# Kernel tuning notes

Hardware: AMD Instinct MI355X
Metric: run time of the kernel (lower is better)

Reference implementation:

```python
import jax, jax.numpy as jnp
import numpy as np
import math

B, H, S, D = 2, 16, 2048, 64


def setup_inputs() -> dict:
    key = jax.random.key(0)
    kq, kk, kv, km = jax.random.split(key, 4)
    query = jax.random.normal(kq, (B, H, S, D), dtype=jnp.float32)
    k_ = jax.random.normal(kk, (B, H, S, D), dtype=jnp.float32)
    value = jax.random.normal(kv, (B, H, S, D), dtype=jnp.float32)
    mask = jax.random.randint(km, (B, 1, S, S), 0, 2).astype(jnp.bool_)
    return {"query": query, "key": k_, "value": value, "mask": mask}


def reference(query, key, value, mask):
    d = query.shape[-1]
    # scores: [B, H, S, S]
    scores = jnp.einsum("bhqd,bhkd->bhqk", query, key) / math.sqrt(d)
    scores = jnp.clip(scores, 1e-09, 1e9)
    # bool-mask branch of the original: masked_fill(mask == False, -1e9)
    scores = jnp.where(mask, scores, jnp.float32(-1e9))
    p_attn = jax.nn.softmax(scores, axis=-1)
    out = jnp.einsum("bhqk,bhkd->bhqd", p_attn, value)
    return out, p_attn
```

## Files before the change

### kernel.cpp

```cpp
#include <hip/hip_runtime.h>


#define B_ 2
#define H_ 16
#define S_ 2048
#define D_ 64
#define BQ 64
#define NQT (S_ / BQ)
#define NCH (S_ / 64)

typedef __attribute__((ext_vector_type(8))) short bf16x8;
typedef __attribute__((ext_vector_type(4))) float f32x4;

__device__ inline short f2bf(float f) {
    unsigned u = __float_as_uint(f);
    u = (u + 0x7FFFu + ((u >> 16) & 1u)) >> 16;
    return (short)u;
}

__device__ __forceinline__ void loadRM(const float* __restrict__ src, int tid, float4* r) {
#pragma unroll
    for (int it = 0; it < 2; ++it) {
        const int g = it * 256 + tid;
        const float4* s4 = reinterpret_cast<const float4*>(src + (g >> 3) * 64 + (g & 7) * 8);
        r[it * 2]     = s4[0];
        r[it * 2 + 1] = s4[1];
    }
}
__device__ __forceinline__ void writeRM(short* dst, int tid, const float4* r) {
#pragma unroll
    for (int it = 0; it < 2; ++it) {
        const int g = it * 256 + tid;
        const int row = g >> 3, b = g & 7;
        const float4 a = r[it * 2], c = r[it * 2 + 1];
        bf16x8 v;
        v[0]=f2bf(a.x); v[1]=f2bf(a.y); v[2]=f2bf(a.z); v[3]=f2bf(a.w);
        v[4]=f2bf(c.x); v[5]=f2bf(c.y); v[6]=f2bf(c.z); v[7]=f2bf(c.w);
        *reinterpret_cast<bf16x8*>(&dst[row * 64 + ((b ^ (row & 7)) << 3)]) = v;
    }
}
__device__ __forceinline__ void loadVc(const float* __restrict__ src, int tid, float* vr) {
    const int d = tid & 63, kq = tid >> 6;
#pragma unroll
    for (int i = 0; i < 16; ++i)
        vr[i] = src[(size_t)(kq * 16 + i) * 64 + d];
}
__device__ __forceinline__ void writeVc(short* dst, int tid, const float* vr) {
    const int d = tid & 63, kq = tid >> 6;
#pragma unroll
    for (int h = 0; h < 2; ++h) {
        bf16x8 v;
#pragma unroll
        for (int i = 0; i < 8; ++i) v[i] = f2bf(vr[h * 8 + i]);
        *reinterpret_cast<bf16x8*>(&dst[d * 64 + (((2 * kq + h) ^ (d & 7)) << 3)]) = v;
    }
}

#define BODY_A(CH, CUR, MVC, MVN)                                              \
  {                                                                            \
    const int ch_ = (CH);                                                      \
    if (ch_ + 1 < NCH) {                                                       \
      _Pragma("unroll") for (int kc = 0; kc < 4; ++kc)                         \
      _Pragma("unroll") for (int j = 0; j < 4; ++j)                            \
        MVN[kc*4+j] = Mb[mrow0 + (size_t)j*S_ + (size_t)(ch_+1)*64 + kc*16 + c16]; \
    }                                                                          \
    __builtin_amdgcn_s_setprio(1);                                             \
    _Pragma("unroll") for (int kc = 0; kc < 4; ++kc) {                         \
      const int kr = kc*16 + c16;                                              \
      bf16x8 kf0 = *(const bf16x8*)&Ks[CUR][kr*64 + ((g16 ^ rsw) << 3)];       \
      bf16x8 kf1 = *(const bf16x8*)&Ks[CUR][kr*64 + (((4+g16) ^ rsw) << 3)];   \
      f32x4 acc = {0.f,0.f,0.f,0.f};                                           \
      acc = __builtin_amdgcn_mfma_f32_16x16x32_bf16(qf0, kf0, acc, 0,0,0);     \
      acc = __builtin_amdgcn_mfma_f32_16x16x32_bf16(qf1, kf1, acc, 0,0,0);     \
      _Pragma("unroll") for (int j = 0; j < 4; ++j) {                          \
        float s = acc[j] * 0.125f;                                             \
        s = fminf(fmaxf(s, 1e-9f), 1e9f);                                      \
        const float e = MVC[kc*4+j] ? __expf(s) : 0.f;                         \
        esum[j] += e;                                                          \
        const int row = g16*4 + j, cg = kc*16 + c16;                           \
        Ps[wv][row*64 + ((cg & 7) | (((cg >> 3) ^ (row & 7)) << 3))] = f2bf(e);\
      }                                                                        \
    }                                                                          \
    _Pragma("unroll") for (int ks = 0; ks < 2; ++ks) {                         \
      bf16x8 pa = *(const bf16x8*)&Ps[wv][c16*64 + (((ks*4+g16) ^ rsw) << 3)]; \
      _Pragma("unroll") for (int dt = 0; dt < 4; ++dt) {                       \
        const int vr_ = dt*16 + c16;                                           \
        bf16x8 vb = *(const bf16x8*)&Vs[CUR][vr_*64 + (((ks*4+g16) ^ (vr_ & 7)) << 3)]; \
        o[dt] = __builtin_amdgcn_mfma_f32_16x16x32_bf16(pa, vb, o[dt], 0,0,0); \
      }                                                                        \
    }                                                                          \
    __builtin_amdgcn_s_setprio(0);                                             \
    {                                                                          \
      unsigned wb = 0;                                                         \
      _Pragma("unroll") for (int i = 0; i < 16; ++i)                           \
        wb |= (MVC[i] != 0 ? 1u : 0u) << i;                                    \
      MBh[tid * 34 + ch_] = (unsigned short)wb;                                \
    }                                                                          \
    if (ch_ + 1 < NCH) { writeRM(Ks[(CUR)^1], tid, kA); writeVc(Vs[(CUR)^1], tid, vA); } \
    if (ch_ + 2 < NCH) { loadRM(Kb + (size_t)(ch_+2)*4096, tid, kA);           \
                         loadVc(Vb + (size_t)(ch_+2)*4096, tid, vA); }         \
    __syncthreads();                                                           \
  }

#define BODY_B(CH, CUR, MKW)                                                   \
  {                                                                            \
    const int ch_ = (CH);                                                      \
    const unsigned mw_ = (MKW);                                                \
    __builtin_amdgcn_s_setprio(1);                                             \
    _Pragma("unroll") for (int kc = 0; kc < 4; ++kc) {                         \
      const int kr = kc*16 + c16;                                              \
      bf16x8 kf0 = *(const bf16x8*)&Ks[CUR][kr*64 + ((g16 ^ rsw) << 3)];       \
      bf16x8 kf1 = *(const bf16x8*)&Ks[CUR][kr*64 + (((4+g16) ^ rsw) << 3)];   \
      f32x4 acc = {0.f,0.f,0.f,0.f};                                           \
      acc = __builtin_amdgcn_mfma_f32_16x16x32_bf16(qf0, kf0, acc, 0,0,0);     \
      acc = __builtin_amdgcn_mfma_f32_16x16x32_bf16(qf1, kf1, acc, 0,0,0);     \
      _Pragma("unroll") for (int j = 0; j < 4; ++j) {                          \
        float s = acc[j] * 0.125f;                                             \
        s = fminf(fmaxf(s, 1e-9f), 1e9f);                                      \
        const float p = ((mw_ >> (kc*4 + j)) & 1u) ? __expf(s) * inv[j] : 0.f; \
        Pg[(size_t)(wv*16 + g16*4 + j)*S_ + (size_t)ch_*64 + kc*16 + c16] = p; \
      }                                                                        \
    }                                                                          \
    __builtin_amdgcn_s_setprio(0);                                             \
    if (ch_ + 1 < NCH) writeRM(Ks[(CUR)^1], tid, kA);                          \
    if (ch_ + 2 < NCH) loadRM(Kb + (size_t)(ch_+2)*4096, tid, kA);             \
    __syncthreads();                                                           \
  }

__global__ __launch_bounds__(256, 2) void attn_fused(
    const float* __restrict__ Q, const float* __restrict__ K,
    const float* __restrict__ V, const int* __restrict__ M,
    float* __restrict__ Out, float* __restrict__ P)
{
    __shared__ short Ks[2][4096];
    __shared__ short Vs[2][4096];
    __shared__ short Ps[4][1024];
    __shared__ unsigned short MBh[256 * 34];

    const int tid  = threadIdx.x;
    const int wv   = tid >> 6;
    const int lane = tid & 63;
    const int g16  = lane >> 4;
    const int c16  = lane & 15;
    const int rsw  = c16 & 7;

    const int wid = (blockIdx.x & 7) * (gridDim.x >> 3) + (blockIdx.x >> 3);
    const int bh = wid >> 5;
    const int qt = wid & 31;
    const int qbase = qt * BQ;

    const float* Qb = Q + ((size_t)bh * S_ + qbase) * D_;
    const float* Kb = K + (size_t)bh * S_ * D_;
    const float* Vb = V + (size_t)bh * S_ * D_;
    const int*   Mb = M + (size_t)(bh >> 4) * S_ * S_;
    float*       Pg = P + ((size_t)bh * S_ + qbase) * S_;
    float*       Og = Out + ((size_t)bh * S_ + qbase) * D_;

    float4 kA[4]; float vA[16];

    {
        float4 qA[4];
        loadRM(Qb, tid, qA);
        loadRM(Kb, tid, kA);
        loadVc(Vb, tid, vA);
        writeRM(&Ps[0][0], tid, qA);
    }
    __syncthreads();
    const int qrow = wv * 16 + c16;
    const short* Qst = &Ps[0][0];
    const bf16x8 qf0 = *(const bf16x8*)&Qst[qrow*64 + ((g16 ^ rsw) << 3)];
    const bf16x8 qf1 = *(const bf16x8*)&Qst[qrow*64 + (((4+g16) ^ rsw) << 3)];
    writeRM(Ks[0], tid, kA);
    writeVc(Vs[0], tid, vA);
    loadRM(Kb + 4096, tid, kA);
    loadVc(Vb + 4096, tid, vA);

    const size_t mrow0 = (size_t)(qbase + wv*16 + g16*4) * S_;
    int mv0[16], mv1[16];
#pragma unroll
    for (int kc = 0; kc < 4; ++kc)
#pragma unroll
        for (int j = 0; j < 4; ++j)
            mv0[kc*4+j] = Mb[mrow0 + (size_t)j*S_ + kc*16 + c16];
    __syncthreads();

    float esum[4] = {0.f, 0.f, 0.f, 0.f};
    f32x4 o[4];
#pragma unroll
    for (int dt = 0; dt < 4; ++dt) o[dt] = f32x4{0.f, 0.f, 0.f, 0.f};

    for (int t = 0; t < NCH/2; ++t) {
        BODY_A(2*t,     0, mv0, mv1)
        BODY_A(2*t + 1, 1, mv1, mv0)
    }

    float inv[4];
#pragma unroll
    for (int j = 0; j < 4; ++j) {
        float v = esum[j];
        v += __shfl_xor(v, 1);
        v += __shfl_xor(v, 2);
        v += __shfl_xor(v, 4);
        v += __shfl_xor(v, 8);
        inv[j] = 1.0f / v;
    }
#pragma unroll
    for (int dt = 0; dt < 4; ++dt)
#pragma unroll
        for (int j = 0; j < 4; ++j)
            Og[(size_t)(wv*16 + g16*4 + j) * D_ + dt*16 + c16] = o[dt][j] * inv[j];

    loadRM(Kb, tid, kA);
    writeRM(Ks[0], tid, kA);
    loadRM(Kb + 4096, tid, kA);
    __syncthreads();

    for (int t = 0; t < NCH/2; ++t) {
        const unsigned w = *(const unsigned*)&MBh[tid * 34 + 2*t];
        BODY_B(2*t,     0, w & 0xffffu)
        BODY_B(2*t + 1, 1, w >> 16)
    }
}

extern "C" void kernel_launch(void* const* d_in, const int* in_sizes, int n_in,
                              void* d_out, int out_size, void* d_ws, size_t ws_size,
                              hipStream_t stream) {
    const float* Q = (const float*)d_in[0];
    const float* K = (const float*)d_in[1];
    const float* V = (const float*)d_in[2];
    const int*   M = (const int*)d_in[3];

    float* Out = (float*)d_out;
    float* P   = (float*)d_out + (size_t)B_ * H_ * S_ * D_;

    hipLaunchKernelGGL(attn_fused, dim3(B_ * H_ * NQT), dim3(256), 0, stream,
                       Q, K, V, M, Out, P);
}
```

Measured before the change: 249.3 us.

## Precompute packed mask bitmask in workspace before fused attention kernel

Adds a pre-pass kernel that packs the int mask into 64-bit ballot words in the workspace. The attention kernel then reads these compact words instead of re-reading int32 mask values from every head's block, and drops the shared-memory mask-bit cache. That cache took about 17KB of LDS, so the launch bound rises to allow 3 blocks per CU. The cost is an extra kernel launch and a full pass over the mask, and a fallback to the old kernel remains when the workspace is too small.

```diff
diff --git a/kernel.cpp b/kernel.cpp
--- a/kernel.cpp
+++ b/kernel.cpp
@@ -8,9 +8,11 @@
 #define BQ 64
 #define NQT (S_ / BQ)
 #define NCH (S_ / 64)
+#define BM_WORDS ((size_t)B_ * S_ * (S_ / 64))
 
 typedef __attribute__((ext_vector_type(8))) short bf16x8;
 typedef __attribute__((ext_vector_type(4))) float f32x4;
+typedef unsigned long long u64;
 
 __device__ inline short f2bf(float f) {
     unsigned u = __float_as_uint(f);
@@ -56,7 +58,178 @@
     }
 }
 
-#define BODY_A(CH, CUR, MVC, MVN)                                              \
+__global__ __launch_bounds__(256, 8) void build_bitmask_ws(const int* __restrict__ M,
+                                                           u64* __restrict__ BM)
+{
+    const unsigned total = (unsigned)B_ * S_ * S_;
+    const unsigned stride = gridDim.x * 256;
+    for (unsigned i = blockIdx.x * 256 + threadIdx.x; i < total; i += stride) {
+        const bool mk = (M[i] != 0);
+        const u64 bal = __ballot(mk);
+        if ((threadIdx.x & 63) == 0) BM[i >> 6] = bal;
+    }
+}
+
+#define BODY_A(CH, CUR, BMC, BMN)                                              \
+  {                                                                            \
+    const int ch_ = (CH);                                                      \
+    if (ch_ + 1 < NCH) {                                                       \
+      _Pragma("unroll") for (int j = 0; j < 4; ++j)                            \
+        BMN[j] = BM[Lbase + (size_t)j * 32 + (ch_ + 1)];                       \
+    }                                                                          \
+    __builtin_amdgcn_s_setprio(1);                                             \
+    _Pragma("unroll") for (int kc = 0; kc < 4; ++kc) {                         \
+      const int kr = kc*16 + c16;                                              \
+      bf16x8 kf0 = *(const bf16x8*)&Ks[CUR][kr*64 + ((g16 ^ rsw) << 3)];       \
+      bf16x8 kf1 = *(const bf16x8*)&Ks[CUR][kr*64 + (((4+g16) ^ rsw) << 3)];   \
+      f32x4 acc = {0.f,0.f,0.f,0.f};                                           \
+      acc = __builtin_amdgcn_mfma_f32_16x16x32_bf16(qf0, kf0, acc, 0,0,0);     \
+      acc = __builtin_amdgcn_mfma_f32_16x16x32_bf16(qf1, kf1, acc, 0,0,0);     \
+      _Pragma("unroll") for (int j = 0; j < 4; ++j) {                          \
+        float s = acc[j] * 0.125f;                                             \
+        s = fminf(fmaxf(s, 1e-9f), 1e9f);                                      \
+        const float e = ((BMC[j] >> (kc*16 + c16)) & 1ULL) ? __expf(s) : 0.f;  \
+        esum[j] += e;                                                          \
+        const int row = g16*4 + j, cg = kc*16 + c16;                           \
+        Ps[wv][row*64 + ((cg & 7) | (((cg >> 3) ^ (row & 7)) << 3))] = f2bf(e);\
+      }                                                                        \
+    }                                                                          \
+    _Pragma("unroll") for (int ks = 0; ks < 2; ++ks) {                         \
+      bf16x8 pa = *(const bf16x8*)&Ps[wv][c16*64 + (((ks*4+g16) ^ rsw) << 3)]; \
+      _Pragma("unroll") for (int dt = 0; dt < 4; ++dt) {                       \
+        const int vr_ = dt*16 + c16;                                           \
+        bf16x8 vb = *(const bf16x8*)&Vs[CUR][vr_*64 + (((ks*4+g16) ^ (vr_ & 7)) << 3)]; \
+        o[dt] = __builtin_amdgcn_mfma_f32_16x16x32_bf16(pa, vb, o[dt], 0,0,0); \
+      }                                                                        \
+    }                                                                          \
+    __builtin_amdgcn_s_setprio(0);                                             \
+    if (ch_ + 1 < NCH) { writeRM(Ks[(CUR)^1], tid, kA); writeVc(Vs[(CUR)^1], tid, vA); } \
+    if (ch_ + 2 < NCH) { loadRM(Kb + (size_t)(ch_+2)*4096, tid, kA);           \
+                         loadVc(Vb + (size_t)(ch_+2)*4096, tid, vA); }         \
+    __syncthreads();                                                           \
+  }
+
+#define BODY_B(CH, CUR, BMC, BMN)                                              \
+  {                                                                            \
+    const int ch_ = (CH);                                                      \
+    if (ch_ + 1 < NCH) {                                                       \
+      _Pragma("unroll") for (int j = 0; j < 4; ++j)                            \
+        BMN[j] = BM[Lbase + (size_t)j * 32 + (ch_ + 1)];                       \
+    }                                                                          \
+    __builtin_amdgcn_s_setprio(1);                                             \
+    _Pragma("unroll") for (int kc = 0; kc < 4; ++kc) {                         \
+      const int kr = kc*16 + c16;                                              \
+      bf16x8 kf0 = *(const bf16x8*)&Ks[CUR][kr*64 + ((g16 ^ rsw) << 3)];       \
+      bf16x8 kf1 = *(const bf16x8*)&Ks[CUR][kr*64 + (((4+g16) ^ rsw) << 3)];   \
+      f32x4 acc = {0.f,0.f,0.f,0.f};                                           \
+      acc = __builtin_amdgcn_mfma_f32_16x16x32_bf16(qf0, kf0, acc, 0,0,0);     \
+      acc = __builtin_amdgcn_mfma_f32_16x16x32_bf16(qf1, kf1, acc, 0,0,0);     \
+      _Pragma("unroll") for (int j = 0; j < 4; ++j) {                          \
+        float s = acc[j] * 0.125f;                                             \
+        s = fminf(fmaxf(s, 1e-9f), 1e9f);                                      \
+        const float p = ((BMC[j] >> (kc*16 + c16)) & 1ULL) ? __expf(s)*inv[j] : 0.f; \
+        Pg[(size_t)(wv*16 + g16*4 + j)*S_ + (size_t)ch_*64 + kc*16 + c16] = p; \
+      }                                                                        \
+    }                                                                          \
+    __builtin_amdgcn_s_setprio(0);                                             \
+    if (ch_ + 1 < NCH) writeRM(Ks[(CUR)^1], tid, kA);                          \
+    if (ch_ + 2 < NCH) loadRM(Kb + (size_t)(ch_+2)*4096, tid, kA);             \
+    __syncthreads();                                                           \
+  }
+
+__global__ __launch_bounds__(256, 3) void attn_bm(
+    const float* __restrict__ Q, const float* __restrict__ K,
+    const float* __restrict__ V, const u64* __restrict__ BM,
+    float* __restrict__ Out, float* __restrict__ P)
+{
+    __shared__ short Ks[2][4096];
+    __shared__ short Vs[2][4096];
+    __shared__ short Ps[4][1024];
+
+    const int tid  = threadIdx.x;
+    const int wv   = tid >> 6;
+    const int lane = tid & 63;
+    const int g16  = lane >> 4;
+    const int c16  = lane & 15;
+    const int rsw  = c16 & 7;
+
+    const int wid = (blockIdx.x & 7) * (gridDim.x >> 3) + (blockIdx.x >> 3);
+    const int bh = wid >> 5;
+    const int qt = wid & 31;
+    const int qbase = qt * BQ;
+
+    const float* Qb = Q + ((size_t)bh * S_ + qbase) * D_;
+    const float* Kb = K + (size_t)bh * S_ * D_;
+    const float* Vb = V + (size_t)bh * S_ * D_;
+    float*       Pg = P + ((size_t)bh * S_ + qbase) * S_;
+    float*       Og = Out + ((size_t)bh * S_ + qbase) * D_;
+
+    const size_t Lbase = ((size_t)(bh >> 4) * S_ + qbase + wv*16 + g16*4) * 32;
+
+    float4 kA[4]; float vA[16];
+
+    {
+        float4 qA[4];
+        loadRM(Qb, tid, qA);
+        loadRM(Kb, tid, kA);
+        loadVc(Vb, tid, vA);
+        writeRM(&Ps[0][0], tid, qA);
+    }
+    __syncthreads();
+    const int qrow = wv * 16 + c16;
+    const short* Qst = &Ps[0][0];
+    const bf16x8 qf0 = *(const bf16x8*)&Qst[qrow*64 + ((g16 ^ rsw) << 3)];
+    const bf16x8 qf1 = *(const bf16x8*)&Qst[qrow*64 + (((4+g16) ^ rsw) << 3)];
+    writeRM(Ks[0], tid, kA);
+    writeVc(Vs[0], tid, vA);
+    loadRM(Kb + 4096, tid, kA);
+    loadVc(Vb + 4096, tid, vA);
+
+    u64 bm0[4], bm1[4];
+#pragma unroll
+    for (int j = 0; j < 4; ++j) bm0[j] = BM[Lbase + (size_t)j * 32];
+    __syncthreads();
+
+    float esum[4] = {0.f, 0.f, 0.f, 0.f};
+    f32x4 o[4];
+#pragma unroll
+    for (int dt = 0; dt < 4; ++dt) o[dt] = f32x4{0.f, 0.f, 0.f, 0.f};
+
+    for (int t = 0; t < NCH/2; ++t) {
+        BODY_A(2*t,     0, bm0, bm1)
+        BODY_A(2*t + 1, 1, bm1, bm0)
+    }
+
+    float inv[4];
+#pragma unroll
+    for (int j = 0; j < 4; ++j) {
+        float v = esum[j];
+        v += __shfl_xor(v, 1);
+        v += __shfl_xor(v, 2);
+        v += __shfl_xor(v, 4);
+        v += __shfl_xor(v, 8);
+        inv[j] = 1.0f / v;
+    }
+#pragma unroll
+    for (int dt = 0; dt < 4; ++dt)
+#pragma unroll
+        for (int j = 0; j < 4; ++j)
+            Og[(size_t)(wv*16 + g16*4 + j) * D_ + dt*16 + c16] = o[dt][j] * inv[j];
+
+    loadRM(Kb, tid, kA);
+#pragma unroll
+    for (int j = 0; j < 4; ++j) bm0[j] = BM[Lbase + (size_t)j * 32];
+    writeRM(Ks[0], tid, kA);
+    loadRM(Kb + 4096, tid, kA);
+    __syncthreads();
+
+    for (int t = 0; t < NCH/2; ++t) {
+        BODY_B(2*t,     0, bm0, bm1)
+        BODY_B(2*t + 1, 1, bm1, bm0)
+    }
+}
+
+#define BODY_AR(CH, CUR, MVC, MVN)                                             \
   {                                                                            \
     const int ch_ = (CH);                                                      \
     if (ch_ + 1 < NCH) {                                                       \
@@ -102,7 +275,7 @@
     __syncthreads();                                                           \
   }
 
-#define BODY_B(CH, CUR, MKW)                                                   \
+#define BODY_BR(CH, CUR, MKW)                                                  \
   {                                                                            \
     const int ch_ = (CH);                                                      \
     const unsigned mw_ = (MKW);                                                \
@@ -127,7 +300,7 @@
     __syncthreads();                                                           \
   }
 
-__global__ __launch_bounds__(256, 2) void attn_fused(
+__global__ __launch_bounds__(256, 2) void attn_fused_raw(
     const float* __restrict__ Q, const float* __restrict__ K,
     const float* __restrict__ V, const int* __restrict__ M,
     float* __restrict__ Out, float* __restrict__ P)
@@ -157,7 +330,6 @@
     float*       Og = Out + ((size_t)bh * S_ + qbase) * D_;
 
     float4 kA[4]; float vA[16];
-
     {
         float4 qA[4];
         loadRM(Qb, tid, qA);
@@ -190,8 +362,8 @@
     for (int dt = 0; dt < 4; ++dt) o[dt] = f32x4{0.f, 0.f, 0.f, 0.f};
 
     for (int t = 0; t < NCH/2; ++t) {
-        BODY_A(2*t,     0, mv0, mv1)
-        BODY_A(2*t + 1, 1, mv1, mv0)
+        BODY_AR(2*t,     0, mv0, mv1)
+        BODY_AR(2*t + 1, 1, mv1, mv0)
     }
 
     float inv[4];
@@ -217,8 +389,8 @@
 
     for (int t = 0; t < NCH/2; ++t) {
         const unsigned w = *(const unsigned*)&MBh[tid * 34 + 2*t];
-        BODY_B(2*t,     0, w & 0xffffu)
-        BODY_B(2*t + 1, 1, w >> 16)
+        BODY_BR(2*t,     0, w & 0xffffu)
+        BODY_BR(2*t + 1, 1, w >> 16)
     }
 }
 
@@ -233,6 +405,13 @@
     float* Out = (float*)d_out;
     float* P   = (float*)d_out + (size_t)B_ * H_ * S_ * D_;
 
-    hipLaunchKernelGGL(attn_fused, dim3(B_ * H_ * NQT), dim3(256), 0, stream,
-                       Q, K, V, M, Out, P);
-}
+    if (ws_size >= BM_WORDS * sizeof(u64)) {
+        u64* BM = (u64*)d_ws;
+        hipLaunchKernelGGL(build_bitmask_ws, dim3(4096), dim3(256), 0, stream, M, BM);
+        hipLaunchKernelGGL(attn_bm, dim3(B_ * H_ * NQT), dim3(256), 0, stream,
+                           Q, K, V, BM, Out, P);
+    } else {
+        hipLaunchKernelGGL(attn_fused_raw, dim3(B_ * H_ * NQT), dim3(256), 0, stream,
+                           Q, K, V, M, Out, P);
+    }
+}
```

New measurement: 400.9 us. +60.8%, slower.

## Keep mask bits in registers instead of LDS and raise occupancy to three blocks

Applied to the files above, without the earlier changes.

The per-thread packed mask bitfield moves out of the shared-memory MBh array into a 16-element register array, and both chunk loops are fully unrolled so that array can stay in registers. Removing about 17 KB of LDS per block, together with launch bounds of 3 blocks per SM, is meant to raise occupancy for this memory-bound kernel. The risk is register pressure from full unrolling plus the extra mbits registers under a tighter VGPR budget, which could cause spills.

```diff
diff --git a/kernel.cpp b/kernel.cpp
--- a/kernel.cpp
+++ b/kernel.cpp
@@ -56,14 +56,16 @@
     }
 }
 
-#define BODY_A(CH, CUR, MVC, MVN)                                              \
+#define BODY_A(CH, CUR)                                                        \
   {                                                                            \
     const int ch_ = (CH);                                                      \
+    int tm[16];                                                                \
     if (ch_ + 1 < NCH) {                                                       \
       _Pragma("unroll") for (int kc = 0; kc < 4; ++kc)                         \
       _Pragma("unroll") for (int j = 0; j < 4; ++j)                            \
-        MVN[kc*4+j] = Mb[mrow0 + (size_t)j*S_ + (size_t)(ch_+1)*64 + kc*16 + c16]; \
-    }                                                                          \
+        tm[kc*4+j] = Mb[mrow0 + (size_t)j*S_ + (size_t)(ch_+1)*64 + kc*16 + c16]; \
+    }                                                                          \
+    const unsigned mw_ = (ch_ & 1) ? (mbits[ch_>>1] >> 16) : (mbits[ch_>>1] & 0xffffu); \
     __builtin_amdgcn_s_setprio(1);                                             \
     _Pragma("unroll") for (int kc = 0; kc < 4; ++kc) {                         \
       const int kr = kc*16 + c16;                                              \
@@ -75,7 +77,7 @@
       _Pragma("unroll") for (int j = 0; j < 4; ++j) {                          \
         float s = acc[j] * 0.125f;                                             \
         s = fminf(fmaxf(s, 1e-9f), 1e9f);                                      \
-        const float e = MVC[kc*4+j] ? __expf(s) : 0.f;                         \
+        const float e = ((mw_ >> (kc*4 + j)) & 1u) ? __expf(s) : 0.f;          \
         esum[j] += e;                                                          \
         const int row = g16*4 + j, cg = kc*16 + c16;                           \
         Ps[wv][row*64 + ((cg & 7) | (((cg >> 3) ^ (row & 7)) << 3))] = f2bf(e);\
@@ -90,22 +92,24 @@
       }                                                                        \
     }                                                                          \
     __builtin_amdgcn_s_setprio(0);                                             \
-    {                                                                          \
+    if (ch_ + 1 < NCH) {                                                       \
       unsigned wb = 0;                                                         \
       _Pragma("unroll") for (int i = 0; i < 16; ++i)                           \
-        wb |= (MVC[i] != 0 ? 1u : 0u) << i;                                    \
-      MBh[tid * 34 + ch_] = (unsigned short)wb;                                \
-    }                                                                          \
-    if (ch_ + 1 < NCH) { writeRM(Ks[(CUR)^1], tid, kA); writeVc(Vs[(CUR)^1], tid, vA); } \
+        wb |= (tm[i] != 0 ? 1u : 0u) << i;                                     \
+      if ((ch_ + 1) & 1) mbits[(ch_+1)>>1] |= (wb << 16);                      \
+      else               mbits[(ch_+1)>>1]  = wb;                              \
+    }                                                                          \
+    if (ch_ + 1 < NCH) { writeRM((short*)Ks[(CUR)^1], tid, kA);                \
+                         writeVc((short*)Vs[(CUR)^1], tid, vA); }              \
     if (ch_ + 2 < NCH) { loadRM(Kb + (size_t)(ch_+2)*4096, tid, kA);           \
                          loadVc(Vb + (size_t)(ch_+2)*4096, tid, vA); }         \
     __syncthreads();                                                           \
   }
 
-#define BODY_B(CH, CUR, MKW)                                                   \
+#define BODY_B(CH, CUR)                                                        \
   {                                                                            \
     const int ch_ = (CH);                                                      \
-    const unsigned mw_ = (MKW);                                                \
+    const unsigned mw_ = (ch_ & 1) ? (mbits[ch_>>1] >> 16) : (mbits[ch_>>1] & 0xffffu); \
     __builtin_amdgcn_s_setprio(1);                                             \
     _Pragma("unroll") for (int kc = 0; kc < 4; ++kc) {                         \
       const int kr = kc*16 + c16;                                              \
@@ -122,12 +126,12 @@
       }                                                                        \
     }                                                                          \
     __builtin_amdgcn_s_setprio(0);                                             \
-    if (ch_ + 1 < NCH) writeRM(Ks[(CUR)^1], tid, kA);                          \
+    if (ch_ + 1 < NCH) writeRM((short*)Ks[(CUR)^1], tid, kA);                  \
     if (ch_ + 2 < NCH) loadRM(Kb + (size_t)(ch_+2)*4096, tid, kA);             \
     __syncthreads();                                                           \
   }
 
-__global__ __launch_bounds__(256, 2) void attn_fused(
+__global__ __launch_bounds__(256, 3) void attn_fused(
     const float* __restrict__ Q, const float* __restrict__ K,
     const float* __restrict__ V, const int* __restrict__ M,
     float* __restrict__ Out, float* __restrict__ P)
@@ -135,7 +139,6 @@
     __shared__ short Ks[2][4096];
     __shared__ short Vs[2][4096];
     __shared__ short Ps[4][1024];
-    __shared__ unsigned short MBh[256 * 34];
 
     const int tid  = threadIdx.x;
     const int wv   = tid >> 6;
@@ -157,6 +160,7 @@
     float*       Og = Out + ((size_t)bh * S_ + qbase) * D_;
 
     float4 kA[4]; float vA[16];
+    unsigned mbits[16];
 
     {
         float4 qA[4];
@@ -170,28 +174,32 @@
     const short* Qst = &Ps[0][0];
     const bf16x8 qf0 = *(const bf16x8*)&Qst[qrow*64 + ((g16 ^ rsw) << 3)];
     const bf16x8 qf1 = *(const bf16x8*)&Qst[qrow*64 + (((4+g16) ^ rsw) << 3)];
-    writeRM(Ks[0], tid, kA);
-    writeVc(Vs[0], tid, vA);
+    writeRM((short*)Ks[0], tid, kA);
+    writeVc((short*)Vs[0], tid, vA);
     loadRM(Kb + 4096, tid, kA);
     loadVc(Vb + 4096, tid, vA);
 
     const size_t mrow0 = (size_t)(qbase + wv*16 + g16*4) * S_;
-    int mv0[16], mv1[16];
-#pragma unroll
-    for (int kc = 0; kc < 4; ++kc)
-#pragma unroll
-        for (int j = 0; j < 4; ++j)
-            mv0[kc*4+j] = Mb[mrow0 + (size_t)j*S_ + kc*16 + c16];
+    {
+        unsigned wb = 0;
+#pragma unroll
+        for (int kc = 0; kc < 4; ++kc)
+#pragma unroll
+            for (int j = 0; j < 4; ++j)
+                wb |= (Mb[mrow0 + (size_t)j*S_ + kc*16 + c16] != 0 ? 1u : 0u) << (kc*4+j);
+        mbits[0] = wb;
+    }
     __syncthreads();
 
     float esum[4] = {0.f, 0.f, 0.f, 0.f};
     f32x4 o[4];
 #pragma unroll
-    for (int dt = 0; dt < 4; ++dt) o[dt] = f32x4{0.f, 0.f, 0.f, 0.f};
-
+    for (int dt = 0; dt < 4; ++dt) o[dt] = f32x4{0.f,0.f,0.f,0.f};
+
+#pragma unroll
     for (int t = 0; t < NCH/2; ++t) {
-        BODY_A(2*t,     0, mv0, mv1)
-        BODY_A(2*t + 1, 1, mv1, mv0)
+        BODY_A(2*t,     0)
+        BODY_A(2*t + 1, 1)
     }
 
     float inv[4];
@@ -211,14 +219,14 @@
             Og[(size_t)(wv*16 + g16*4 + j) * D_ + dt*16 + c16] = o[dt][j] * inv[j];
 
     loadRM(Kb, tid, kA);
-    writeRM(Ks[0], tid, kA);
+    writeRM((short*)Ks[0], tid, kA);
     loadRM(Kb + 4096, tid, kA);
     __syncthreads();
 
+#pragma unroll
     for (int t = 0; t < NCH/2; ++t) {
-        const unsigned w = *(const unsigned*)&MBh[tid * 34 + 2*t];
-        BODY_B(2*t,     0, w & 0xffffu)
-        BODY_B(2*t + 1, 1, w >> 16)
+        BODY_B(2*t,     0)
+        BODY_B(2*t + 1, 1)
     }
 }
 
```

Measured after the change: 534.1 us. 114% more time.

## Single-buffer K/V shared tiles and raise occupancy to four blocks per CU

Applied to the files above, without the earlier changes.

Replaces the double-buffered K/V shared-memory tiles with single buffers. Each chunk is now written to LDS, synchronized, and then the next chunk is prefetched into registers. The mask-bit table drops its padding from 34 to 32 entries per thread, and launch bounds request four blocks per SM instead of two. The aim is to cut LDS use and register pressure so more blocks run concurrently. The cost is an extra barrier per chunk, less overlap between LDS writes and compute, and possible LDS bank conflicts from removing the padding.

```diff
diff --git a/kernel.cpp b/kernel.cpp
--- a/kernel.cpp
+++ b/kernel.cpp
@@ -56,10 +56,14 @@
     }
 }
 
-#define BODY_A(CH, CUR, MVC, MVN)                                              \
+#define BODY_A(CH, MVC, MVN)                                                   \
   {                                                                            \
     const int ch_ = (CH);                                                      \
-    if (ch_ + 1 < NCH) {                                                       \
+    writeRM(Ks, tid, kA);                           \
+    writeVc(Vs, tid, vA);                                                      \
+    __syncthreads();                                        \
+    if (ch_ + 1 < NCH) { loadRM(Kb + (size_t)(ch_+1)*4096, tid, kA);           \
+                         loadVc(Vb + (size_t)(ch_+1)*4096, tid, vA);           \
       _Pragma("unroll") for (int kc = 0; kc < 4; ++kc)                         \
       _Pragma("unroll") for (int j = 0; j < 4; ++j)                            \
         MVN[kc*4+j] = Mb[mrow0 + (size_t)j*S_ + (size_t)(ch_+1)*64 + kc*16 + c16]; \
@@ -67,8 +71,8 @@
     __builtin_amdgcn_s_setprio(1);                                             \
     _Pragma("unroll") for (int kc = 0; kc < 4; ++kc) {                         \
       const int kr = kc*16 + c16;                                              \
-      bf16x8 kf0 = *(const bf16x8*)&Ks[CUR][kr*64 + ((g16 ^ rsw) << 3)];       \
-      bf16x8 kf1 = *(const bf16x8*)&Ks[CUR][kr*64 + (((4+g16) ^ rsw) << 3)];   \
+      bf16x8 kf0 = *(const bf16x8*)&Ks[kr*64 + ((g16 ^ rsw) << 3)];            \
+      bf16x8 kf1 = *(const bf16x8*)&Ks[kr*64 + (((4+g16) ^ rsw) << 3)];        \
       f32x4 acc = {0.f,0.f,0.f,0.f};                                           \
       acc = __builtin_amdgcn_mfma_f32_16x16x32_bf16(qf0, kf0, acc, 0,0,0);     \
       acc = __builtin_amdgcn_mfma_f32_16x16x32_bf16(qf1, kf1, acc, 0,0,0);     \
@@ -85,7 +89,7 @@
       bf16x8 pa = *(const bf16x8*)&Ps[wv][c16*64 + (((ks*4+g16) ^ rsw) << 3)]; \
       _Pragma("unroll") for (int dt = 0; dt < 4; ++dt) {                       \
         const int vr_ = dt*16 + c16;                                           \
-        bf16x8 vb = *(const bf16x8*)&Vs[CUR][vr_*64 + (((ks*4+g16) ^ (vr_ & 7)) << 3)]; \
+        bf16x8 vb = *(const bf16x8*)&Vs[vr_*64 + (((ks*4+g16) ^ (vr_ & 7)) << 3)]; \
         o[dt] = __builtin_amdgcn_mfma_f32_16x16x32_bf16(pa, vb, o[dt], 0,0,0); \
       }                                                                        \
     }                                                                          \
@@ -94,23 +98,23 @@
       unsigned wb = 0;                                                         \
       _Pragma("unroll") for (int i = 0; i < 16; ++i)                           \
         wb |= (MVC[i] != 0 ? 1u : 0u) << i;                                    \
-      MBh[tid * 34 + ch_] = (unsigned short)wb;                                \
-    }                                                                          \
-    if (ch_ + 1 < NCH) { writeRM(Ks[(CUR)^1], tid, kA); writeVc(Vs[(CUR)^1], tid, vA); } \
-    if (ch_ + 2 < NCH) { loadRM(Kb + (size_t)(ch_+2)*4096, tid, kA);           \
-                         loadVc(Vb + (size_t)(ch_+2)*4096, tid, vA); }         \
-    __syncthreads();                                                           \
+      MBh[tid * 32 + ch_] = (unsigned short)wb;                                \
+    }                                                                          \
+    __syncthreads();                      \
   }
 
-#define BODY_B(CH, CUR, MKW)                                                   \
+#define BODY_B(CH, MKW)                                                        \
   {                                                                            \
     const int ch_ = (CH);                                                      \
+    writeRM(Ks, tid, kA);                                                      \
+    __syncthreads();                                                           \
+    if (ch_ + 1 < NCH) loadRM(Kb + (size_t)(ch_+1)*4096, tid, kA);             \
     const unsigned mw_ = (MKW);                                                \
     __builtin_amdgcn_s_setprio(1);                                             \
     _Pragma("unroll") for (int kc = 0; kc < 4; ++kc) {                         \
       const int kr = kc*16 + c16;                                              \
-      bf16x8 kf0 = *(const bf16x8*)&Ks[CUR][kr*64 + ((g16 ^ rsw) << 3)];       \
-      bf16x8 kf1 = *(const bf16x8*)&Ks[CUR][kr*64 + (((4+g16) ^ rsw) << 3)];   \
+      bf16x8 kf0 = *(const bf16x8*)&Ks[kr*64 + ((g16 ^ rsw) << 3)];            \
+      bf16x8 kf1 = *(const bf16x8*)&Ks[kr*64 + (((4+g16) ^ rsw) << 3)];        \
       f32x4 acc = {0.f,0.f,0.f,0.f};                                           \
       acc = __builtin_amdgcn_mfma_f32_16x16x32_bf16(qf0, kf0, acc, 0,0,0);     \
       acc = __builtin_amdgcn_mfma_f32_16x16x32_bf16(qf1, kf1, acc, 0,0,0);     \
@@ -122,20 +126,18 @@
       }                                                                        \
     }                                                                          \
     __builtin_amdgcn_s_setprio(0);                                             \
-    if (ch_ + 1 < NCH) writeRM(Ks[(CUR)^1], tid, kA);                          \
-    if (ch_ + 2 < NCH) loadRM(Kb + (size_t)(ch_+2)*4096, tid, kA);             \
     __syncthreads();                                                           \
   }
 
-__global__ __launch_bounds__(256, 2) void attn_fused(
+__global__ __launch_bounds__(256, 4) void attn_fused(
     const float* __restrict__ Q, const float* __restrict__ K,
     const float* __restrict__ V, const int* __restrict__ M,
     float* __restrict__ Out, float* __restrict__ P)
 {
-    __shared__ short Ks[2][4096];
-    __shared__ short Vs[2][4096];
+    __shared__ short Ks[4096];
+    __shared__ short Vs[4096];
     __shared__ short Ps[4][1024];
-    __shared__ unsigned short MBh[256 * 34];
+    __shared__ unsigned short MBh[256 * 32];
 
     const int tid  = threadIdx.x;
     const int wv   = tid >> 6;
@@ -170,10 +172,6 @@
     const short* Qst = &Ps[0][0];
     const bf16x8 qf0 = *(const bf16x8*)&Qst[qrow*64 + ((g16 ^ rsw) << 3)];
     const bf16x8 qf1 = *(const bf16x8*)&Qst[qrow*64 + (((4+g16) ^ rsw) << 3)];
-    writeRM(Ks[0], tid, kA);
-    writeVc(Vs[0], tid, vA);
-    loadRM(Kb + 4096, tid, kA);
-    loadVc(Vb + 4096, tid, vA);
 
     const size_t mrow0 = (size_t)(qbase + wv*16 + g16*4) * S_;
     int mv0[16], mv1[16];
@@ -190,8 +188,8 @@
     for (int dt = 0; dt < 4; ++dt) o[dt] = f32x4{0.f, 0.f, 0.f, 0.f};
 
     for (int t = 0; t < NCH/2; ++t) {
-        BODY_A(2*t,     0, mv0, mv1)
-        BODY_A(2*t + 1, 1, mv1, mv0)
+        BODY_A(2*t,     mv0, mv1)
+        BODY_A(2*t + 1, mv1, mv0)
     }
 
     float inv[4];
@@ -211,14 +209,11 @@
             Og[(size_t)(wv*16 + g16*4 + j) * D_ + dt*16 + c16] = o[dt][j] * inv[j];
 
     loadRM(Kb, tid, kA);
-    writeRM(Ks[0], tid, kA);
-    loadRM(Kb + 4096, tid, kA);
-    __syncthreads();
 
     for (int t = 0; t < NCH/2; ++t) {
-        const unsigned w = *(const unsigned*)&MBh[tid * 34 + 2*t];
-        BODY_B(2*t,     0, w & 0xffffu)
-        BODY_B(2*t + 1, 1, w >> 16)
+        const unsigned w = *(const unsigned*)&MBh[tid * 32 + 2*t];
+        BODY_B(2*t,     w & 0xffffu)
+        BODY_B(2*t + 1, w >> 16)
     }
 }
 
```

After: 676.9 us. 171% more time.
